# Optimization experiments

Hardware: AMD Instinct MI355X
Metric: run time of the kernel (lower is better)

Reference implementation:

```python
import jax, jax.numpy as jnp
import numpy as np

# dims
D = 1024; H = 16; DH = D // H; FF = 4096; E = 4; K = 64; M = 256; B = 2; S = 1024
DEPTH = 1.0 + 12.0 / 24.0 * 0.5  # depth_factor for layer_idx=12, num_layers=24
SCALE = 1.0 / np.sqrt(DH)
GATE_DIM = 128


def _heads(t):
    # (B,S,D) -> (B,H,S,DH)
    return t.reshape(t.shape[0], t.shape[1], H, DH).transpose(0, 2, 1, 3)


def _merge(t):
    # (B,H,S,DH) -> (B,S,D)
    return t.transpose(0, 2, 1, 3).reshape(t.shape[0], t.shape[2], D)


def _ln(x, g, b):
    mu = x.mean(-1, keepdims=True)
    var = x.var(-1, keepdims=True)
    return (x - mu) / jnp.sqrt(var + 1e-5) * g + b


def _mha(x, wq, bq, wk, bk, wv, bv, wo, bo):
    q = _heads(x @ wq + bq); k = _heads(x @ wk + bk); v = _heads(x @ wv + bv)
    s = jnp.einsum('bhqd,bhkd->bhqk', q, k) * SCALE
    a = jax.nn.softmax(s, axis=-1)
    return _merge(jnp.einsum('bhqk,bhkd->bhqd', a, v)) @ wo + bo


def _sparse_mha(x, wq, bq, wk, bk, wv, bv, wo, bo):
    # DynamicSparseAttention: keep top-K scores per query, mask the rest
    q = _heads(x @ wq + bq); k = _heads(x @ wk + bk); v = _heads(x @ wv + bv)
    s = jnp.einsum('bhqd,bhkd->bhqk', q, k) * SCALE
    thr = jax.lax.top_k(s, K)[0][..., -1:]             # kth-largest per query
    s = jnp.where(s >= thr, s, -1e9)
    a = jax.nn.softmax(s, axis=-1)
    return _merge(jnp.einsum('bhqk,bhkd->bhqd', a, v)) @ wo + bo


def _performer(x, wq, bq, wk, bk, wv, bv, wo, bo, wf):
    # LearnedPerformerAttention: learned ReLU feature maps, linear attention
    q = _heads(x @ wq + bq); k = _heads(x @ wk + bk); v = _heads(x @ wv + bv)
    pq = jax.nn.relu(jnp.einsum('bhsd,dm->bhsm', q, wf))
    pk = jax.nn.relu(jnp.einsum('bhsd,dm->bhsm', k, wf))
    kv = jnp.einsum('bhsm,bhsd->bhmd', pk, v)          # (B,H,M,DH)
    z = pk.sum(axis=2)                                  # (B,H,M)
    num = jnp.einsum('bhsm,bhmd->bhsd', pq, kv)
    den = jnp.einsum('bhsm,bhm->bhs', pq, z) + 1e-6
    return _merge(num / den[..., None]) @ wo + bo


def setup_inputs() -> dict:
    key = jax.random.key(0)
    ks = iter(jax.random.split(key, 64))

    def w(shape):
        fan_in = shape[-2] if len(shape) > 1 else shape[-1]
        return (jax.random.normal(next(ks), shape, jnp.float32) / np.sqrt(fan_in))

    inp = {'x': jax.random.normal(next(ks), (B, S, D), jnp.float32)}
    # AdaptiveReasoningGate
    inp['arg_w1'] = w((D, GATE_DIM)); inp['arg_b1'] = jnp.zeros(GATE_DIM)
    inp['arg_w2'] = w((GATE_DIM, 2)); inp['arg_b2'] = jnp.zeros(2)
    # MoE attention: router + per-expert MHA
    inp['moe_wr'] = w((D, E)); inp['moe_br'] = jnp.zeros(E)
    for n in ('wq', 'wk', 'wv', 'wo'):
        inp['moe_' + n] = w((E, D, D))
        inp['moe_b' + n[1]] = jnp.zeros((E, D))
    # sparse attention
    for n in ('wq', 'wk', 'wv', 'wo'):
        inp['sp_' + n] = w((D, D)); inp['sp_b' + n[1]] = jnp.zeros(D)
    # performer attention
    for n in ('wq', 'wk', 'wv', 'wo'):
        inp['pf_' + n] = w((D, D)); inp['pf_b' + n[1]] = jnp.zeros(D)
    inp['pf_wf'] = w((DH, M))
    # TAA gate, attention combiner gate
    inp['taa_wg'] = w((D, 2)); inp['taa_bg'] = jnp.zeros(2)
    inp['ag_w'] = w((D, 2)); inp['ag_b'] = jnp.zeros(2)
    # FFN
    inp['ffn_w1'] = w((D, FF)); inp['ffn_b1'] = jnp.zeros(FF)
    inp['ffn_w2'] = w((FF, D)); inp['ffn_b2'] = jnp.zeros(D)
    # norms
    for i in (1, 2, 3):
        inp[f'n{i}_g'] = jnp.ones(D); inp[f'n{i}_b'] = jnp.zeros(D)
    return inp


def _forward(x, arg_w1, arg_b1, arg_w2, arg_b2,
             moe_wr, moe_br, moe_wq, moe_bq, moe_wk, moe_bk, moe_wv, moe_bv, moe_wo, moe_bo,
             sp_wq, sp_bq, sp_wk, sp_bk, sp_wv, sp_bv, sp_wo, sp_bo,
             pf_wq, pf_bq, pf_wk, pf_bk, pf_wv, pf_bv, pf_wo, pf_bo, pf_wf,
             taa_wg, taa_bg, ag_w, ag_b,
             ffn_w1, ffn_b1, ffn_w2, ffn_b2,
             n1_g, n1_b, n2_g, n2_b, n3_g, n3_b):
    avg = x.mean(axis=1)  # (B,D)
    # AdaptiveReasoningGate (attn_weight computed but unused in original forward)
    gw = jax.nn.sigmoid(jax.nn.gelu(avg @ arg_w1 + arg_b1) @ arg_w2 + arg_b2)
    ffn_weight = gw[:, 1][:, None, None]
    # MoE attention: token-level softmax routing over E expert MHAs
    ex_out = jax.vmap(
        lambda wq, bq, wk, bk, wv, bv, wo, bo: _mha(x, wq, bq, wk, bk, wv, bv, wo, bo)
    )(moe_wq, moe_bq, moe_wk, moe_bk, moe_wv, moe_bv, moe_wo, moe_bo)  # (E,B,S,D)
    gates = jax.nn.softmax(x @ moe_wr + moe_br, axis=-1)               # (B,S,E)
    moe_out = jnp.einsum('ebsd,bse->bsd', ex_out, gates)
    # Hybrid thought-aware attention (dropout = identity, eval mode)
    sp = _sparse_mha(x, sp_wq, sp_bq, sp_wk, sp_bk, sp_wv, sp_bv, sp_wo, sp_bo)
    pf = _performer(x, pf_wq, pf_bq, pf_wk, pf_bk, pf_wv, pf_bv, pf_wo, pf_bo, pf_wf)
    tg = jax.nn.softmax(avg @ taa_wg + taa_bg, axis=-1)
    taa_out = tg[:, 0][:, None, None] * sp + tg[:, 1][:, None, None] * pf
    # gated combine of MoE and TAA paths
    ag = jax.nn.softmax(avg @ ag_w + ag_b, axis=-1)
    attn_out = (ag[:, 0][:, None, None] * moe_out + ag[:, 1][:, None, None] * taa_out) * DEPTH
    x1 = _ln(x + attn_out, n1_g, n1_b)
    ffn_out = (jax.nn.gelu(x1 @ ffn_w1 + ffn_b1) @ ffn_w2 + ffn_b2) * ffn_weight * DEPTH
    x2 = _ln(x1 + ffn_out, n2_g, n2_b)
    return _ln(x2, n3_g, n3_b)


def reference(x, arg_w1, arg_b1, arg_w2, arg_b2,
              moe_wr, moe_br, moe_wq, moe_bq, moe_wk, moe_bk, moe_wv, moe_bv, moe_wo, moe_bo,
              sp_wq, sp_bq, sp_wk, sp_bk, sp_wv, sp_bv, sp_wo, sp_bo,
              pf_wq, pf_bq, pf_wk, pf_bk, pf_wv, pf_bv, pf_wo, pf_bo, pf_wf,
              taa_wg, taa_bg, ag_w, ag_b,
              ffn_w1, ffn_b1, ffn_w2, ffn_b2,
              n1_g, n1_b, n2_g, n2_b, n3_g, n3_b):
    return _forward(x, arg_w1, arg_b1, arg_w2, arg_b2,
                    moe_wr, moe_br, moe_wq, moe_bq, moe_wk, moe_bk, moe_wv, moe_bv, moe_wo, moe_bo,
                    sp_wq, sp_bq, sp_wk, sp_bk, sp_wv, sp_bv, sp_wo, sp_bo,
                    pf_wq, pf_bq, pf_wk, pf_bk, pf_wv, pf_bv, pf_wo, pf_bo, pf_wf,
                    taa_wg, taa_bg, ag_w, ag_b,
                    ffn_w1, ffn_b1, ffn_w2, ffn_b2,
                    n1_g, n1_b, n2_g, n2_b, n3_g, n3_b)
```

## Files before the change

### kernel.cpp

```cpp
#include <hip/hip_runtime.h>
#include <hip/hip_bf16.h>
#include <math.h>

#define Bq 2
#define Sq 1024
#define Dq 1024
#define Hq 16
#define DHq 64
#define FFq 4096
#define Eq 4
#define Kq 64
#define Mq 256
#define GATEq 128
#define BSq (Bq*Sq)
#define DEPTHF 1.25f
#define SCALEF 0.125f
#define DD (Dq*Dq)
#define PLANE ((size_t)BSq*Dq)

typedef __hip_bfloat16 bf16;
typedef __attribute__((ext_vector_type(8))) __bf16 bf16x8;
typedef __attribute__((ext_vector_type(4))) float f32x4;

__device__ __forceinline__ float toF(float v){ return v; }
__device__ __forceinline__ float toF(bf16 v){ return __bfloat162float(v); }
__device__ __forceinline__ void stF(float* p, size_t i, float v){ p[i] = v; }
__device__ __forceinline__ void stF(bf16* p, size_t i, float v){ p[i] = __float2bfloat16(v); }
__device__ __forceinline__ float gelu_f(float x){
  const float c = 0.7978845608028654f;
  return 0.5f*x*(1.0f + tanhf(c*(x + 0.044715f*x*x*x)));
}
__device__ __forceinline__ unsigned short bfb(float f){
  bf16 h = __float2bfloat16(f);
  return *(unsigned short*)&h;
}
__device__ __forceinline__ float thr_decode(unsigned c){
  unsigned ub = (c & 0x80000000u) ? (c & 0x7FFFFFFFu) : ~c;
  return __uint_as_float(ub);
}
__device__ __forceinline__ void async_lds16(const void* g, void* lds) {
  __builtin_amdgcn_global_load_lds(
      (const __attribute__((address_space(1))) void*)(unsigned long long)(uintptr_t)g,
      (__attribute__((address_space(3))) void*)(unsigned)(uintptr_t)lds, 16, 0, 0);
}

__global__ __launch_bounds__(256)
void detect_kernel(const unsigned* __restrict__ xw, int* __restrict__ flag)
{
  __shared__ int cnt;
  if (threadIdx.x == 0) cnt = 0;
  __syncthreads();
  int c = 0;
  for (int i = threadIdx.x; i < 4096; i += 256) {
    unsigned e = (xw[i] >> 7) & 0xFFu;
    c += (e >= 0x70u && e <= 0x8Fu) ? 1 : 0;
  }
#pragma unroll
  for (int o = 32; o >= 1; o >>= 1) c += __shfl_xor(c, o);
  if ((threadIdx.x & 63) == 0) atomicAdd(&cnt, c);
  __syncthreads();
  if (threadIdx.x == 0) *flag = (cnt > 2048) ? 1 : 0;
}

__global__ __launch_bounds__(256)
void conv_x_kernel(const int* __restrict__ flag, const void* __restrict__ x, bf16* __restrict__ xb)
{
  int f = *flag;
  int i0 = (blockIdx.x*256 + threadIdx.x)*4;
  if (i0 >= BSq*Dq) return;
  if (f) {
    const bf16* s = (const bf16*)x;
#pragma unroll
    for (int k=0;k<4;k++) xb[i0+k] = s[i0+k];
  } else {
    const float* s = (const float*)x;
#pragma unroll
    for (int k=0;k<4;k++) xb[i0+k] = __float2bfloat16(s[i0+k]);
  }
}

template<typename IT>
__device__ void packseg(bf16* dst, const IT* src, int len)
{
  for (int i = threadIdx.x; i < len; i += 256) dst[i] = __float2bfloat16(toF(src[i]));
}
__global__ __launch_bounds__(256)
void pack_bias_kernel(const int* __restrict__ flag, bf16* arena,
    const void* bq, const void* bk, const void* bv, const void* bo,
    const void* sq, const void* sk, const void* sv, const void* so,
    const void* pq, const void* pk, const void* pv, const void* po,
    const void* f1, const void* f2)
{
  int f = *flag;
  if (f) {
    packseg(arena+0,     (const bf16*)bq, 4096); packseg(arena+4096,  (const bf16*)bk, 4096);
    packseg(arena+8192,  (const bf16*)bv, 4096); packseg(arena+12288, (const bf16*)bo, 4096);
    packseg(arena+16384, (const bf16*)sq, 1024); packseg(arena+17408, (const bf16*)sk, 1024);
    packseg(arena+18432, (const bf16*)sv, 1024); packseg(arena+19456, (const bf16*)so, 1024);
    packseg(arena+20480, (const bf16*)pq, 1024); packseg(arena+21504, (const bf16*)pk, 1024);
    packseg(arena+22528, (const bf16*)pv, 1024); packseg(arena+23552, (const bf16*)po, 1024);
    packseg(arena+24576, (const bf16*)f1, 4096); packseg(arena+28672, (const bf16*)f2, 1024);
  } else {
    packseg(arena+0,     (const float*)bq, 4096); packseg(arena+4096,  (const float*)bk, 4096);
    packseg(arena+8192,  (const float*)bv, 4096); packseg(arena+12288, (const float*)bo, 4096);
    packseg(arena+16384, (const float*)sq, 1024); packseg(arena+17408, (const float*)sk, 1024);
    packseg(arena+18432, (const float*)sv, 1024); packseg(arena+19456, (const float*)so, 1024);
    packseg(arena+20480, (const float*)pq, 1024); packseg(arena+21504, (const float*)pk, 1024);
    packseg(arena+22528, (const float*)pv, 1024); packseg(arena+23552, (const float*)po, 1024);
    packseg(arena+24576, (const float*)f1, 4096); packseg(arena+28672, (const float*)f2, 1024);
  }
}

template<typename IT>
__device__ void packwft_body(const IT* __restrict__ wf, bf16* __restrict__ wft)
{
  int i = blockIdx.x*256 + threadIdx.x;
  if (i >= DHq*Mq) return;
  int d = i >> 8, m = i & 255;
  wft[m*DHq + d] = __float2bfloat16(toF(wf[(size_t)d*Mq + m]));
}
__global__ __launch_bounds__(256)
void pack_wft_kernel(const int* __restrict__ flag, const void* wf, bf16* wft)
{
  if (*flag) packwft_body<bf16>((const bf16*)wf, wft);
  else       packwft_body<float>((const float*)wf, wft);
}

template<typename WT>
__device__ void gemm_core(bf16* As, unsigned* Bs,
    const bf16* __restrict__ A, int lda, const WT* __restrict__ W,
    const bf16* __restrict__ barena, int biasOff,
    const float* __restrict__ rowscale, bf16* __restrict__ C,
    float* __restrict__ Cf, int N, int K, int act)
{
  int tid = threadIdx.x;
  int lane = tid & 63, wave = tid >> 6;
  int wr = wave >> 1, wc = wave & 1;
  int bm = blockIdx.x * 128, bn = blockIdx.y * 128;

  int arow1 = wave*16 + (lane>>2);
  int akey = (arow1 >> 1) & 3;
  int acol = ((lane & 3) ^ akey) * 8;
  const bf16* aP1 = A + (size_t)(bm + arow1)*lda + acol;
  const bf16* aP2 = A + (size_t)(bm + arow1 + 64)*lda + acol;

  int kp = tid >> 4, nb8 = (tid & 15)*8;
  const WT* wP = W + (size_t)(2*kp)*N + bn + nb8;

  f32x4 acc[4][4];
#pragma unroll
  for (int i=0;i<4;i++)
#pragma unroll
    for (int j=0;j<4;j++) acc[i][j] = (f32x4){0.f,0.f,0.f,0.f};

  int m = lane & 15, q = lane >> 4;
  int akey2 = (m >> 1) & 3;
  int aq = (q ^ akey2) * 8;

  const int T = K >> 5;
  uint4 rwa, rwb, rwc, rwd;

  async_lds16(aP1, As + wave*512);
  async_lds16(aP2, As + (wave+4)*512);
  aP1 += 32; aP2 += 32;
  if constexpr (sizeof(WT) == 2) {
    rwa = *(const uint4*)wP;
    rwb = *(const uint4*)(wP + N);
  } else {
    const float* f0 = (const float*)wP;
    const float* f1 = (const float*)(wP + N);
    rwa = *(const uint4*)f0; rwb = *(const uint4*)(f0+4);
    rwc = *(const uint4*)f1; rwd = *(const uint4*)(f1+4);
  }
  wP += (size_t)32*N;

  for (int t = 0; t < T; t++) {
    int cur = t & 1;
    unsigned p[8];
    if constexpr (sizeof(WT) == 2) {
      p[0] = (rwa.x & 0xFFFFu) | (rwb.x << 16);  p[1] = (rwa.x >> 16) | (rwb.x & 0xFFFF0000u);
      p[2] = (rwa.y & 0xFFFFu) | (rwb.y << 16);  p[3] = (rwa.y >> 16) | (rwb.y & 0xFFFF0000u);
      p[4] = (rwa.z & 0xFFFFu) | (rwb.z << 16);  p[5] = (rwa.z >> 16) | (rwb.z & 0xFFFF0000u);
      p[6] = (rwa.w & 0xFFFFu) | (rwb.w << 16);  p[7] = (rwa.w >> 16) | (rwb.w & 0xFFFF0000u);
    } else {
      p[0] = (unsigned)bfb(__uint_as_float(rwa.x)) | ((unsigned)bfb(__uint_as_float(rwc.x)) << 16);
      p[1] = (unsigned)bfb(__uint_as_float(rwa.y)) | ((unsigned)bfb(__uint_as_float(rwc.y)) << 16);
      p[2] = (unsigned)bfb(__uint_as_float(rwa.z)) | ((unsigned)bfb(__uint_as_float(rwc.z)) << 16);
      p[3] = (unsigned)bfb(__uint_as_float(rwa.w)) | ((unsigned)bfb(__uint_as_float(rwc.w)) << 16);
      p[4] = (unsigned)bfb(__uint_as_float(rwb.x)) | ((unsigned)bfb(__uint_as_float(rwd.x)) << 16);
      p[5] = (unsigned)bfb(__uint_as_float(rwb.y)) | ((unsigned)bfb(__uint_as_float(rwd.y)) << 16);
      p[6] = (unsigned)bfb(__uint_as_float(rwb.z)) | ((unsigned)bfb(__uint_as_float(rwd.z)) << 16);
      p[7] = (unsigned)bfb(__uint_as_float(rwb.w)) | ((unsigned)bfb(__uint_as_float(rwd.w)) << 16);
    }
    unsigned* bD = Bs + cur*2112 + kp*132 + nb8;
    *(uint4*)(bD)     = make_uint4(p[0],p[1],p[2],p[3]);
    *(uint4*)(bD + 4) = make_uint4(p[4],p[5],p[6],p[7]);
    asm volatile("s_waitcnt vmcnt(0)" ::: "memory");
    __syncthreads();
    if (t + 1 < T) {
      bf16* asn = As + ((t+1)&1)*4096;
      async_lds16(aP1, asn + wave*512);
      async_lds16(aP2, asn + (wave+4)*512);
      aP1 += 32; aP2 += 32;
      if constexpr (sizeof(WT) == 2) {
        rwa = *(const uint4*)wP;
        rwb = *(const uint4*)(wP + N);
      } else {
        const float* f0 = (const float*)wP;
        const float* f1 = (const float*)(wP + N);
        rwa = *(const uint4*)f0; rwb = *(const uint4*)(f0+4);
        rwc = *(const uint4*)f1; rwd = *(const uint4*)(f1+4);
      }
      wP += (size_t)32*N;
    }
    const bf16* asc = As + cur*4096;
    const unsigned* bsc = Bs + cur*2112;
    bf16x8 av[4], bv[4];
#pragma unroll
    for (int i=0;i<4;i++)
      av[i] = *(const bf16x8*)&asc[(wr*64 + i*16 + m)*32 + aq];
#pragma unroll
    for (int j=0;j<4;j++) {
      int n = wc*64 + j*16 + m;
      unsigned b0 = bsc[(q*4+0)*132 + n];
      unsigned b1 = bsc[(q*4+1)*132 + n];
      unsigned b2 = bsc[(q*4+2)*132 + n];
      unsigned b3 = bsc[(q*4+3)*132 + n];
      uint4 bb = make_uint4(b0,b1,b2,b3);
      bv[j] = *(const bf16x8*)&bb;
    }
#pragma unroll
    for (int i=0;i<4;i++)
#pragma unroll
      for (int j=0;j<4;j++)
        acc[i][j] = __builtin_amdgcn_mfma_f32_16x16x32_bf16(av[i], bv[j], acc[i][j], 0, 0, 0);
  }

#pragma unroll
  for (int i=0;i<4;i++) {
    int row0 = bm + wr*64 + i*16 + q*4;
#pragma unroll
    for (int j=0;j<4;j++) {
      int col = bn + wc*64 + j*16 + m;
      float bvv = barena ? toF(barena[biasOff + col]) : 0.f;
#pragma unroll
      for (int r=0;r<4;r++) {
        size_t idx = (size_t)(row0 + r)*N + col;
        if (Cf) {
          Cf[idx] = acc[i][j][r];
        } else {
          float v = acc[i][j][r] + bvv;
          if (act) v = gelu_f(v);
          if (rowscale) v *= rowscale[row0 + r];
          C[idx] = __float2bfloat16(v);
        }
      }
    }
  }
}

__global__ __launch_bounds__(256, 3)
void gemm6_k(const int* __restrict__ flag, const bf16* Abase, long az,
    const void* w0, const void* w1, const void* w2,
    const void* w3, const void* w4, const void* w5,
    long e0, long e1, long e2, long e3, long e4, long e5,
    int b0, int b1, int b2, int b3, int b4, int b5,
    const float* r0, const float* r1, const float* r2,
    const float* r3, const float* r4, const float* r5,
    bf16* c0, bf16* c1, bf16* c2, bf16* c3, bf16* c4, bf16* c5,
    const bf16* barena, int N, int K)
{
  __shared__ bf16 As[2*4096];
  __shared__ unsigned Bs[2*2112];
  int z = blockIdx.z;
  const void* Wp = (z==0)?w0:(z==1)?w1:(z==2)?w2:(z==3)?w3:(z==4)?w4:w5;
  long eo        = (z==0)?e0:(z==1)?e1:(z==2)?e2:(z==3)?e3:(z==4)?e4:e5;
  int bo         = (z==0)?b0:(z==1)?b1:(z==2)?b2:(z==3)?b3:(z==4)?b4:b5;
  const float* rs= (z==0)?r0:(z==1)?r1:(z==2)?r2:(z==3)?r3:(z==4)?r4:r5;
  bf16* C        = (z==0)?c0:(z==1)?c1:(z==2)?c2:(z==3)?c3:(z==4)?c4:c5;
  const bf16* A  = Abase + (size_t)z*az;
  if (*flag) gemm_core<bf16>(As, Bs, A, K, (const bf16*)Wp + eo, barena, bo, rs, C, nullptr, N, K, 0);
  else       gemm_core<float>(As, Bs, A, K, (const float*)Wp + eo, barena, bo, rs, C, nullptr, N, K, 0);
}

__global__ __launch_bounds__(256, 3)
void gemm1_k(const int* __restrict__ flag, const bf16* A, int lda, const void* W,
             const bf16* barena, int biasOff, const float* rowscale,
             bf16* C, float* Cf, long cfz, int N, int K, int act, int kz)
{
  __shared__ bf16 As[2*4096];
  __shared__ unsigned Bs[2*2112];
  int z = blockIdx.z;
  const bf16* Az = A + (size_t)z*kz;
  long wo = (size_t)z*kz*N;
  float* Cfz = Cf ? (Cf + (size_t)z*cfz) : nullptr;
  if (*flag) gemm_core<bf16>(As, Bs, Az, lda, (const bf16*)W + wo, barena, biasOff, rowscale, C, Cfz, N, K, act);
  else       gemm_core<float>(As, Bs, Az, lda, (const float*)W + wo, barena, biasOff, rowscale, C, Cfz, N, K, act);
}

__global__ __launch_bounds__(256)
void combine_ffn2(const float* __restrict__ pf, const bf16* __restrict__ barena,
                  const float* __restrict__ rs, bf16* __restrict__ out)
{
  int i0 = (blockIdx.x*256 + threadIdx.x)*4;
  float4 s0 = *(const float4*)(pf + i0);
  float4 s1 = *(const float4*)(pf + PLANE + i0);
  float4 s2 = *(const float4*)(pf + 2*PLANE + i0);
  float4 s3 = *(const float4*)(pf + 3*PLANE + i0);
  int row = i0 >> 10, col = i0 & 1023;
  float r = rs[row];
  out[i0+0] = __float2bfloat16((s0.x+s1.x+s2.x+s3.x + toF(barena[28672+col+0])) * r);
  out[i0+1] = __float2bfloat16((s0.y+s1.y+s2.y+s3.y + toF(barena[28672+col+1])) * r);
  out[i0+2] = __float2bfloat16((s0.z+s1.z+s2.z+s3.z + toF(barena[28672+col+2])) * r);
  out[i0+3] = __float2bfloat16((s0.w+s1.w+s2.w+s3.w + toF(barena[28672+col+3])) * r);
}

__global__ __launch_bounds__(256)
void vtrans_kernel(const bf16* __restrict__ Vb, long vz, bf16* __restrict__ Vtb, long vtz)
{
  __shared__ bf16 t[64][72];
  const bf16* V = Vb + (size_t)blockIdx.z*vz;
  bf16* Vt = Vtb + (size_t)blockIdx.z*vtz;
  int bh = blockIdx.x;
  int sc_ = blockIdx.y;
  int b = bh >> 4, h = bh & 15;
  int tid = threadIdx.x;
  {
    int s = tid >> 2, dd = (tid & 3) * 16;
    const bf16* src = &V[((size_t)b*Sq + sc_*64 + s)*Dq + h*64 + dd];
    uint4 a0 = *(const uint4*)src;
    uint4 a1 = *(const uint4*)(src + 8);
    *(uint4*)&t[s][dd]     = a0;
    *(uint4*)&t[s][dd + 8] = a1;
  }
  __syncthreads();
  {
    int d = tid >> 2, sp = (tid & 3) * 16;
    unsigned short buf[16];
#pragma unroll
    for (int e = 0; e < 16; e++) {
      bf16 v = t[sp + e][d];
      buf[e] = *(unsigned short*)&v;
    }
    bf16* dst = &Vt[((size_t)bh*DHq + d)*Sq + sc_*64 + sp];
    *(uint4*)dst       = *(uint4*)&buf[0];
    *(uint4*)(dst + 8) = *(uint4*)&buf[8];
  }
}

template<int SPARSE>
__global__ __launch_bounds__(256, 4)
void attn_kernel(const bf16* __restrict__ Q, const bf16* __restrict__ K,
                 const bf16* __restrict__ Vt, bf16* __restrict__ O)
{
  const int PAST = 1032;
  __shared__ bf16 pa[16*PAST];
  __shared__ float partA[64], partB[64];
  __shared__ int cntb[2][64];

  int p_ = blockIdx.x;
  int g_ = (p_ & 7)*4 + ((p_ >> 3) & 3);
  int rb = p_ >> 5;
  int h  = g_ & 15;
  int b  = g_ >> 4;
  int tid = threadIdx.x, lane = tid & 63, wave = tid >> 6;
  int m = lane & 15, q = lane >> 4;
  size_t base = ((size_t)b*Sq)*Dq + (size_t)h*DHq;
  int q0 = rb*16;

  const bf16* qrow = &Q[base + (size_t)(q0+m)*Dq + q*8];
  bf16x8 aq0 = *(const bf16x8*)qrow;
  bf16x8 aq1 = *(const bf16x8*)(qrow + 32);

  f32x4 cc[16];
#pragma unroll
  for (int t = 0; t < 16; t++) {
    int j0 = wave*256 + t*16;
    const bf16* kp = &K[base + (size_t)(j0+m)*Dq + q*8];
    bf16x8 b0 = *(const bf16x8*)kp;
    bf16x8 b1 = *(const bf16x8*)(kp + 32);
    f32x4 c = {0.f,0.f,0.f,0.f};
    c = __builtin_amdgcn_mfma_f32_16x16x32_bf16(aq0, b0, c, 0, 0, 0);
    c = __builtin_amdgcn_mfma_f32_16x16x32_bf16(aq1, b1, c, 0, 0, 0);
#pragma unroll
    for (int r=0;r<4;r++) c[r] *= SCALEF;
    cc[t] = c;
  }

  unsigned lo[4] = {0u,0u,0u,0u};
  if (SPARSE) {
    int cnt_cur[4] = {Sq, Sq, Sq, Sq};
    for (int bit = 31; bit >= 0; bit--) {
      int par = bit & 1;
      unsigned cand[4];
      float candf[4];
      int c4[4] = {0,0,0,0};
#pragma unroll
      for (int r=0;r<4;r++) {
        cand[r] = lo[r] | (1u << bit);
        candf[r] = thr_decode(cand[r]);
      }
#pragma unroll
      for (int t=0;t<16;t++)
#pragma unroll
        for (int r=0;r<4;r++) c4[r] += (cc[t][r] >= candf[r]) ? 1 : 0;
#pragma unroll
      for (int o=1;o<16;o<<=1)
#pragma unroll
        for (int r=0;r<4;r++) c4[r] += __shfl_xor(c4[r], o);
      if (m == 0) {
#pragma unroll
        for (int r=0;r<4;r++) cntb[par][wave*16 + q*4 + r] = c4[r];
      }
      __syncthreads();
      int done = 1;
#pragma unroll
      for (int r=0;r<4;r++) {
        int row = q*4 + r;
        int tot = cntb[par][row] + cntb[par][16+row] + cntb[par][32+row] + cntb[par][48+row];
        if (tot >= Kq) { lo[r] = cand[r]; cnt_cur[r] = tot; }
        done &= (cnt_cur[r] == Kq) ? 1 : 0;
      }
      done &= __shfl_xor(done, 16);
      done &= __shfl_xor(done, 32);
      if (done) break;
    }
  }

  float mrow[4];
#pragma unroll
  for (int r=0;r<4;r++) {
    float v = -1e30f;
#pragma unroll
    for (int t=0;t<16;t++) v = fmaxf(v, cc[t][r]);
#pragma unroll
    for (int o=1;o<16;o<<=1) v = fmaxf(v, __shfl_xor(v, o));
    mrow[r] = v;
  }
  if (m == 0) {
#pragma unroll
    for (int r=0;r<4;r++) partA[wave*16 + q*4 + r] = mrow[r];
  }
  __syncthreads();
#pragma unroll
  for (int r=0;r<4;r++) {
    int row = q*4 + r;
    mrow[r] = fmaxf(fmaxf(partA[row], partA[16+row]), fmaxf(partA[32+row], partA[48+row]));
  }

  float thrf[4];
  if (SPARSE) {
#pragma unroll
    for (int r=0;r<4;r++) {
      thrf[r] = (!(lo[r] & 0x80000000u) && lo[r] <= 0x007FFFFFu)
                    ? -INFINITY : thr_decode(lo[r]);
    }
  }
  float rsum[4] = {0.f,0.f,0.f,0.f};
#pragma unroll
  for (int t=0;t<16;t++) {
    int col = wave*256 + t*16 + m;
#pragma unroll
    for (int r=0;r<4;r++) {
      float p;
      if (SPARSE) p = (cc[t][r] >= thrf[r]) ? __expf(cc[t][r] - mrow[r]) : 0.f;
      else        p = __expf(cc[t][r] - mrow[r]);
      rsum[r] += p;
      pa[(q*4+r)*PAST + col] = __float2bfloat16(p);
    }
  }
#pragma unroll
  for (int r=0;r<4;r++)
#pragma unroll
    for (int o=1;o<16;o<<=1) rsum[r] += __shfl_xor(rsum[r], o);
  if (m == 0) {
#pragma unroll
    for (int r=0;r<4;r++) partB[wave*16 + q*4 + r] = rsum[r];
  }
  __syncthreads();
#pragma unroll
  for (int r=0;r<4;r++) {
    int row = q*4 + r;
    rsum[r] = partB[row] + partB[16+row] + partB[32+row] + partB[48+row];
    rsum[r] = fmaxf(rsum[r], 1e-30f);
  }

  const bf16* vtp = &Vt[((size_t)(b*Hq + h)*DHq + wave*16 + m)*Sq];
  f32x4 oc = {0.f,0.f,0.f,0.f};
#pragma unroll 8
  for (int ks = 0; ks < 32; ks++) {
    bf16x8 af = *(const bf16x8*)&pa[m*PAST + ks*32 + q*8];
    bf16x8 bv = *(const bf16x8*)&vtp[ks*32 + q*8];
    oc = __builtin_amdgcn_mfma_f32_16x16x32_bf16(af, bv, oc, 0, 0, 0);
  }
#pragma unroll
  for (int r=0;r<4;r++) {
    O[base + (size_t)(q0 + q*4 + r)*Dq + wave*16 + m] = __float2bfloat16(oc[r] / rsum[r]);
  }
}

__global__ __launch_bounds__(256)
void perf_kv_mfma(const bf16* __restrict__ Kb, const bf16* __restrict__ Vt,
                  const bf16* __restrict__ wft, bf16* __restrict__ kvb,
                  float* __restrict__ zg)
{
  __shared__ bf16 pbuf[4][32*40];
  __shared__ float kvred[4][64*32];
  __shared__ float zred[4][32];

  int bh = blockIdx.x;
  int mg = blockIdx.y;
  int b = bh >> 4, h = bh & 15;
  int tid = threadIdx.x, lane = tid & 63, wave = tid >> 6;
  int ml = lane & 15, q = lane >> 4;
  size_t kbase = ((size_t)b*Sq)*Dq + (size_t)h*DHq;
  const bf16* vtb = Vt + (size_t)bh*DHq*Sq;
  int sw0 = wave*256;
  bf16* pw = pbuf[wave];

  bf16x8 awf[2][2];
#pragma unroll
  for (int t=0;t<2;t++) {
    const bf16* p = &wft[(size_t)(mg*32 + t*16 + ml)*DHq + q*8];
    awf[t][0] = *(const bf16x8*)p;
    awf[t][1] = *(const bf16x8*)(p + 32);
  }

  f32x4 acc[4][2];
#pragma unroll
  for (int dt=0;dt<4;dt++)
#pragma unroll
    for (int t=0;t<2;t++) acc[dt][t] = (f32x4){0.f,0.f,0.f,0.f};
  float zacc[2][4] = {{0.f,0.f,0.f,0.f},{0.f,0.f,0.f,0.f}};

  for (int st = 0; st < 8; st++) {
    int s0 = sw0 + st*32;
    f32x4 pk[2][2];
#pragma unroll
    for (int sc=0;sc<2;sc++) {
      const bf16* kp = &Kb[kbase + (size_t)(s0 + sc*16 + ml)*Dq + q*8];
      bf16x8 b0 = *(const bf16x8*)kp;
      bf16x8 b1 = *(const bf16x8*)(kp + 32);
#pragma unroll
      for (int t=0;t<2;t++) {
        f32x4 c = (f32x4){0.f,0.f,0.f,0.f};
        c = __builtin_amdgcn_mfma_f32_16x16x32_bf16(awf[t][0], b0, c, 0, 0, 0);
        c = __builtin_amdgcn_mfma_f32_16x16x32_bf16(awf[t][1], b1, c, 0, 0, 0);
        pk[t][sc] = c;
      }
    }
#pragma unroll
    for (int t=0;t<2;t++)
#pragma unroll
      for (int sc=0;sc<2;sc++)
#pragma unroll
        for (int r=0;r<4;r++) {
          float v = fmaxf(pk[t][sc][r], 0.f);
          zacc[t][r] += v;
          pw[(t*16 + q*4 + r)*40 + sc*16 + ml] = __float2bfloat16(v);
        }
#pragma unroll
    for (int dt=0;dt<4;dt++) {
      bf16x8 av = *(const bf16x8*)&vtb[(size_t)(dt*16 + ml)*Sq + s0 + q*8];
#pragma unroll
      for (int t=0;t<2;t++) {
        bf16x8 bp = *(const bf16x8*)&pw[(t*16 + ml)*40 + q*8];
        acc[dt][t] = __builtin_amdgcn_mfma_f32_16x16x32_bf16(av, bp, acc[dt][t], 0, 0, 0);
      }
    }
  }

#pragma unroll
  for (int dt=0;dt<4;dt++)
#pragma unroll
    for (int t=0;t<2;t++)
#pragma unroll
      for (int r=0;r<4;r++)
        kvred[wave][(dt*16 + q*4 + r)*32 + t*16 + ml] = acc[dt][t][r];
#pragma unroll
  for (int t=0;t<2;t++)
#pragma unroll
    for (int r=0;r<4;r++) {
      float v = zacc[t][r];
#pragma unroll
      for (int o=1;o<16;o<<=1) v += __shfl_xor(v, o);
      if (ml == 0) zred[wave][t*16 + q*4 + r] = v;
    }
  __syncthreads();
  for (int p = tid; p < 2048; p += 256) {
    float s = kvred[0][p] + kvred[1][p] + kvred[2][p] + kvred[3][p];
    int d = p >> 5, mloc = p & 31;
    kvb[(size_t)bh*(DHq*Mq) + d*Mq + mg*32 + mloc] = __float2bfloat16(s);
  }
  if (tid < 32) {
    float s = zred[0][tid] + zred[1][tid] + zred[2][tid] + zred[3][tid];
    zg[bh*Mq + mg*32 + tid] = s;
  }
}

__global__ __launch_bounds__(256)
void perf_out_mfma(const bf16* __restrict__ Q, const bf16* __restrict__ wft,
                   const bf16* __restrict__ kvb, const float* __restrict__ zg,
                   bf16* __restrict__ O)
{
  const int PQST = 264;
  __shared__ bf16 pa2[64*PQST];
  __shared__ float zs[Mq];

  int blk = blockIdx.x;
  int sc_ = blk & 15;
  int bh  = blk >> 4;
  int b = bh >> 4, h = bh & 15;
  int tid = threadIdx.x, lane = tid & 63, wave = tid >> 6;
  int ml = lane & 15, q = lane >> 4;
  size_t base = ((size_t)b*Sq)*Dq + (size_t)h*DHq;
  int s0 = sc_*64;

  zs[tid] = zg[bh*Mq + tid];

  const bf16* qp = &Q[base + (size_t)(s0 + wave*16 + ml)*Dq + q*8];
  bf16x8 aq0 = *(const bf16x8*)qp;
  bf16x8 aq1 = *(const bf16x8*)(qp + 32);
  __syncthreads();

  f32x4 pq[16];
#pragma unroll
  for (int mt=0;mt<16;mt++) {
    const bf16* wp = &wft[(size_t)(mt*16 + ml)*DHq + q*8];
    bf16x8 b0 = *(const bf16x8*)wp;
    bf16x8 b1 = *(const bf16x8*)(wp + 32);
    f32x4 c = (f32x4){0.f,0.f,0.f,0.f};
    c = __builtin_amdgcn_mfma_f32_16x16x32_bf16(aq0, b0, c, 0, 0, 0);
    c = __builtin_amdgcn_mfma_f32_16x16x32_bf16(aq1, b1, c, 0, 0, 0);
    pq[mt] = c;
  }

  float den[4] = {1e-6f, 1e-6f, 1e-6f, 1e-6f};
#pragma unroll
  for (int mt=0;mt<16;mt++)
#pragma unroll
    for (int r=0;r<4;r++) {
      float v = fmaxf(pq[mt][r], 0.f);
      den[r] += v * zs[mt*16 + ml];
      pa2[(wave*16 + q*4 + r)*PQST + mt*16 + ml] = __float2bfloat16(v);
    }
#pragma unroll
  for (int r=0;r<4;r++)
#pragma unroll
    for (int o=1;o<16;o<<=1) den[r] += __shfl_xor(den[r], o);
  __syncthreads();

  const bf16* kvp = kvb + (size_t)bh*(DHq*Mq);
  f32x4 oc[4];
#pragma unroll
  for (int dt=0;dt<4;dt++) oc[dt] = (f32x4){0.f,0.f,0.f,0.f};
#pragma unroll
  for (int ks=0; ks<8; ks++) {
    bf16x8 ap = *(const bf16x8*)&pa2[(wave*16 + ml)*PQST + ks*32 + q*8];
#pragma unroll
    for (int dt=0;dt<4;dt++) {
      bf16x8 bk = *(const bf16x8*)&kvp[(size_t)(dt*16 + ml)*Mq + ks*32 + q*8];
      oc[dt] = __builtin_amdgcn_mfma_f32_16x16x32_bf16(ap, bk, oc[dt], 0, 0, 0);
    }
  }
#pragma unroll
  for (int dt=0;dt<4;dt++)
#pragma unroll
    for (int r=0;r<4;r++)
      O[base + (size_t)(s0 + wave*16 + q*4 + r)*Dq + dt*16 + ml] =
          __float2bfloat16(oc[dt][r] / den[r]);
}

template<typename IT>
__device__ void ln_body(float* buf, float* red, const IT* __restrict__ xb,
                        const void* Ap, const void* Bp,
                        const IT* __restrict__ g, const IT* __restrict__ be,
                        void* out, int mode)
{
  int row = blockIdx.x;
  int tid = threadIdx.x;
  size_t off = (size_t)row*Dq;
  for (int dd = tid; dd < Dq; dd += 256) {
    float v;
    if (mode == 0)      v = toF(xb[off+dd]) + toF(((const bf16*)Ap)[off+dd]);
    else if (mode == 1) v = toF(((const bf16*)Ap)[off+dd]) + toF(((const bf16*)Bp)[off+dd]);
    else if (mode == 3) {
      const bf16* P = (const bf16*)Ap;
      v = toF(xb[off+dd]);
#pragma unroll
      for (int p=0;p<6;p++) v += toF(P[(size_t)p*PLANE + off + dd]);
    }
    else                v = toF(((const bf16*)Ap)[off+dd]);
    buf[dd] = v;
  }
  __syncthreads();
  float s = 0.f, q = 0.f;
  for (int dd = tid; dd < Dq; dd += 256) { float v = buf[dd]; s += v; q += v*v; }
#pragma unroll
  for (int o=32;o>=1;o>>=1) { s += __shfl_xor(s,o); q += __shfl_xor(q,o); }
  int w = tid >> 6;
  if ((tid & 63) == 0) { red[w] = s; red[4+w] = q; }
  __syncthreads();
  if (tid == 0) {
    float S1 = red[0]+red[1]+red[2]+red[3];
    float Q1 = red[4]+red[5]+red[6]+red[7];
    float mu = S1 / (float)Dq;
    float var = Q1 / (float)Dq - mu*mu;
    red[8] = mu; red[9] = rsqrtf(fmaxf(var, 0.f) + 1e-5f);
  }
  __syncthreads();
  float mu = red[8], inv = red[9];
  for (int dd = tid; dd < Dq; dd += 256) {
    float v = (buf[dd]-mu)*inv*toF(g[dd]) + toF(be[dd]);
    if (mode == 2) stF((IT*)out, off+dd, v);
    else           stF((bf16*)out, off+dd, v);
  }
}

__global__ __launch_bounds__(256)
void ln_kernel(const int* __restrict__ flag, const void* xb, const void* A, const void* Bv,
               const void* g, const void* be, void* out, int mode)
{
  __shared__ float buf[Dq];
  __shared__ float red[10];
  if (*flag) ln_body<bf16>(buf, red, (const bf16*)xb, A, Bv, (const bf16*)g, (const bf16*)be, out, mode);
  else       ln_body<float>(buf, red, (const float*)xb, A, Bv, (const float*)g, (const float*)be, out, mode);
}

__global__ __launch_bounds__(256)
void avg2_kernel(const int* __restrict__ flag, const void* __restrict__ x, float* __restrict__ avgsum)
{
  int b  = blockIdx.x >> 4;
  int sc = blockIdx.x & 15;
  int t = threadIdx.x;
  int c0 = t*4;
  float a0=0.f,a1=0.f,a2=0.f,a3=0.f;
  if (*flag) {
    const unsigned* X = (const unsigned*)x;
    for (int s = sc*64; s < sc*64+64; s++) {
      size_t bi = (((size_t)(b*Sq + s))*Dq + c0) >> 1;
      unsigned u0 = X[bi], u1 = X[bi+1];
      a0 += __uint_as_float(u0 << 16);
      a1 += __uint_as_float(u0 & 0xFFFF0000u);
      a2 += __uint_as_float(u1 << 16);
      a3 += __uint_as_float(u1 & 0xFFFF0000u);
    }
  } else {
    const float* X = (const float*)x;
    for (int s = sc*64; s < sc*64+64; s++) {
      float4 v = *(const float4*)&X[((size_t)(b*Sq + s))*Dq + c0];
      a0 += v.x; a1 += v.y; a2 += v.z; a3 += v.w;
    }
  }
  atomicAdd(&avgsum[b*Dq + c0 + 0], a0);
  atomicAdd(&avgsum[b*Dq + c0 + 1], a1);
  atomicAdd(&avgsum[b*Dq + c0 + 2], a2);
  atomicAdd(&avgsum[b*Dq + c0 + 3], a3);
}

template<typename IT>
__device__ void gdots_body(const float* __restrict__ avgs,
    const IT* __restrict__ w1, const IT* __restrict__ b1,
    const IT* __restrict__ taw, const IT* __restrict__ tab,
    const IT* __restrict__ agw, const IT* __restrict__ agb,
    float* __restrict__ g1b, float* __restrict__ lgb)
{
  int blk = blockIdx.x;
  int tid = threadIdx.x, lane = tid & 63, wave = tid >> 6;
  if (blk < 64) {
    int o = blk*4 + wave;
    int bb = o >> 7, j = o & 127;
    const float* av = avgs + bb*Dq;
    float a = 0.f;
#pragma unroll
    for (int k = 0; k < 16; k++) {
      int dd = k*64 + lane;
      a += av[dd] * toF(w1[dd*GATEq + j]);
    }
#pragma unroll
    for (int off=32; off>=1; off>>=1) a += __shfl_xor(a, off);
    if (lane == 0) g1b[o] = gelu_f(a*(1.f/(float)Sq) + toF(b1[j]));
  } else {
    int bb = wave >> 1, c = wave & 1;
    const float* av = avgs + bb*Dq;
    const IT* wm = (blk == 64) ? taw : agw;
    const IT* bm = (blk == 64) ? tab : agb;
    float a = 0.f;
#pragma unroll
    for (int k = 0; k < 16; k++) {
      int dd = k*64 + lane;
      a += av[dd] * toF(wm[dd*2 + c]);
    }
#pragma unroll
    for (int off=32; off>=1; off>>=1) a += __shfl_xor(a, off);
    if (lane == 0) lgb[(blk-64)*4 + wave] = a*(1.f/(float)Sq) + toF(bm[c]);
  }
}
__global__ __launch_bounds__(256)
void gate_dots_kernel(const int* __restrict__ flag, const float* avgs,
    const void* w1, const void* b1, const void* taw, const void* tab,
    const void* agw, const void* agb, float* g1b, float* lgb)
{
  if (*flag) gdots_body<bf16>(avgs, (const bf16*)w1,(const bf16*)b1,(const bf16*)taw,
      (const bf16*)tab,(const bf16*)agw,(const bf16*)agb, g1b, lgb);
  else gdots_body<float>(avgs, (const float*)w1,(const float*)b1,(const float*)taw,
      (const float*)tab,(const float*)agw,(const float*)agb, g1b, lgb);
}

template<typename IT>
__device__ void gfin_body(float* sh, const float* __restrict__ g1b, const float* __restrict__ lgb,
    const IT* __restrict__ w2, const IT* __restrict__ b2,
    float* __restrict__ cmb0, float* __restrict__ rs_tg0,
    float* __restrict__ rs_tg1, float* __restrict__ rs_ffn)
{
  int tid = threadIdx.x, lane = tid & 63, wave = tid >> 6;
  if (wave < 2) {
    float a = g1b[wave*128 + lane] * toF(w2[lane*2 + 1])
            + g1b[wave*128 + 64 + lane] * toF(w2[(64+lane)*2 + 1]);
#pragma unroll
    for (int off=32; off>=1; off>>=1) a += __shfl_xor(a, off);
    if (lane == 0) sh[wave] = 1.f/(1.f + __expf(-(a + toF(b2[1]))));
  }
  __syncthreads();
  if (tid < Bq) {
    int b = tid;
    float t0 = lgb[b*2], t1 = lgb[b*2+1];
    float m = fmaxf(t0,t1);
    float e0=__expf(t0-m), e1=__expf(t1-m), inv=1.f/(e0+e1);
    float tg0 = e0*inv, tg1 = e1*inv;
    float a0 = lgb[4+b*2], a1l = lgb[4+b*2+1];
    m = fmaxf(a0,a1l);
    float f0=__expf(a0-m), f1=__expf(a1l-m); inv = 1.f/(f0+f1);
    float ag0 = f0*inv, ag1 = f1*inv;
    cmb0[b] = ag0*DEPTHF;
    sh[2+b] = tg0*ag1*DEPTHF;
    sh[4+b] = tg1*ag1*DEPTHF;
    sh[6+b] = sh[b]*DEPTHF;
  }
  __syncthreads();
  for (int i = tid; i < BSq; i += 256) {
    int b = i >> 10;
    rs_tg0[i] = sh[2+b]; rs_tg1[i] = sh[4+b]; rs_ffn[i] = sh[6+b];
  }
}
__global__ __launch_bounds__(256)
void gate_fin_kernel(const int* __restrict__ flag, const float* g1b, const float* lgb,
    const void* w2, const void* b2, float* cmb0,
    float* rs_tg0, float* rs_tg1, float* rs_ffn)
{
  __shared__ float sh[8];
  if (*flag) gfin_body<bf16>(sh, g1b, lgb, (const bf16*)w2, (const bf16*)b2, cmb0, rs_tg0, rs_tg1, rs_ffn);
  else       gfin_body<float>(sh, g1b, lgb, (const float*)w2, (const float*)b2, cmb0, rs_tg0, rs_tg1, rs_ffn);
}

template<typename IT>
__device__ void router_body(const IT* __restrict__ x, const IT* __restrict__ wr,
                            const IT* __restrict__ br, const float* __restrict__ cmb0,
                            float* __restrict__ gates_t)
{
  int row = blockIdx.x;
  int tid = threadIdx.x;
  size_t off = (size_t)row*Dq;
  float a0=0,a1=0,a2=0,a3=0;
  for (int dd = tid; dd < Dq; dd += 64) {
    float xv = toF(x[off+dd]);
    a0 += xv*toF(wr[dd*Eq+0]);
    a1 += xv*toF(wr[dd*Eq+1]);
    a2 += xv*toF(wr[dd*Eq+2]);
    a3 += xv*toF(wr[dd*Eq+3]);
  }
#pragma unroll
  for (int o=32;o>=1;o>>=1) {
    a0 += __shfl_xor(a0,o); a1 += __shfl_xor(a1,o);
    a2 += __shfl_xor(a2,o); a3 += __shfl_xor(a3,o);
  }
  if (tid == 0) {
    a0 += toF(br[0]); a1 += toF(br[1]); a2 += toF(br[2]); a3 += toF(br[3]);
    float m = fmaxf(fmaxf(a0,a1),fmaxf(a2,a3));
    float e0=__expf(a0-m), e1=__expf(a1-m), e2=__expf(a2-m), e3=__expf(a3-m);
    float inv = 1.f/(e0+e1+e2+e3);
    float sc = cmb0[row >> 10];
    gates_t[0*BSq+row]=e0*inv*sc; gates_t[1*BSq+row]=e1*inv*sc;
    gates_t[2*BSq+row]=e2*inv*sc; gates_t[3*BSq+row]=e3*inv*sc;
  }
}
__global__ __launch_bounds__(64)
void router_kernel(const int* __restrict__ flag, const void* x, const void* wr,
                   const void* br, const float* cmb0, float* gates_t)
{
  if (*flag) router_body<bf16>((const bf16*)x, (const bf16*)wr, (const bf16*)br, cmb0, gates_t);
  else       router_body<float>((const float*)x, (const float*)wr, (const float*)br, cmb0, gates_t);
}

extern "C" void kernel_launch(void* const* d_in, const int* in_sizes, int n_in,
                              void* d_out, int out_size, void* d_ws, size_t ws_size,
                              hipStream_t stream) {
  const void* x      = d_in[0];
  const void* arg_w1 = d_in[1];  const void* arg_b1 = d_in[2];
  const void* arg_w2 = d_in[3];  const void* arg_b2 = d_in[4];
  const void* moe_wr = d_in[5];  const void* moe_br = d_in[6];
  const void* moe_wq = d_in[7];  const void* moe_bq = d_in[8];
  const void* moe_wk = d_in[9];  const void* moe_bk = d_in[10];
  const void* moe_wv = d_in[11]; const void* moe_bv = d_in[12];
  const void* moe_wo = d_in[13]; const void* moe_bo = d_in[14];
  const void* sp_wq  = d_in[15]; const void* sp_bq  = d_in[16];
  const void* sp_wk  = d_in[17]; const void* sp_bk  = d_in[18];
  const void* sp_wv  = d_in[19]; const void* sp_bv  = d_in[20];
  const void* sp_wo  = d_in[21]; const void* sp_bo  = d_in[22];
  const void* pf_wq  = d_in[23]; const void* pf_bq  = d_in[24];
  const void* pf_wk  = d_in[25]; const void* pf_bk  = d_in[26];
  const void* pf_wv  = d_in[27]; const void* pf_bv  = d_in[28];
  const void* pf_wo  = d_in[29]; const void* pf_bo  = d_in[30];
  const void* pf_wf  = d_in[31];
  const void* taa_wg = d_in[32]; const void* taa_bg = d_in[33];
  const void* ag_w   = d_in[34]; const void* ag_b   = d_in[35];
  const void* ffn_w1 = d_in[36]; const void* ffn_b1 = d_in[37];
  const void* ffn_w2 = d_in[38]; const void* ffn_b2 = d_in[39];
  const void* n1_g   = d_in[40]; const void* n1_b   = d_in[41];
  const void* n2_g   = d_in[42]; const void* n2_b   = d_in[43];
  const void* n3_g   = d_in[44]; const void* n3_b   = d_in[45];

  char* w = (char*)d_ws;
  const size_t MB = 1024*1024;
  bf16* xb  = (bf16*)w;
  bf16* Qp  = (bf16*)(w + 4*MB);
  bf16* KV  = (bf16*)(w + 28*MB);
  bf16* Vt  = (bf16*)(w + 44*MB);
  bf16* Pp  = (bf16*)(w + 28*MB);
  bf16* x1    = (bf16*)(w + 4*MB);
  bf16* ffn_h = (bf16*)(w + 8*MB);
  float* partF= (float*)(w + 24*MB);
  bf16* tmpb  = (bf16*)w;
  bf16* x2    = (bf16*)w;
  char* book = w + 56*MB;
  float* rs_tg0 = (float*)book;
  float* rs_tg1 = rs_tg0 + BSq;
  float* rs_ffn = rs_tg1 + BSq;
  float* cmb0   = rs_ffn + BSq;
  float* avgp   = cmb0 + 16;
  float* gates_t= avgp + Bq*Dq;
  float* zb     = gates_t + Eq*BSq;
  float* g1b    = zb + Bq*Hq*Mq;
  float* lgb    = g1b + 256;
  int*   dflag  = (int*)(lgb + 8);
  bf16*  barena = (bf16*)(dflag + 16);
  bf16*  wft    = barena + 29696;
  bf16*  kvb    = (bf16*)(w + 57*MB);

  detect_kernel<<<1, 256, 0, stream>>>((const unsigned*)x, dflag);
  hipMemsetAsync(avgp, 0, (size_t)(Bq*Dq)*sizeof(float), stream);
  conv_x_kernel<<<BSq*Dq/1024, 256, 0, stream>>>(dflag, x, xb);
  pack_bias_kernel<<<1, 256, 0, stream>>>(dflag, barena,
      moe_bq, moe_bk, moe_bv, moe_bo, sp_bq, sp_bk, sp_bv, sp_bo,
      pf_bq, pf_bk, pf_bv, pf_bo, ffn_b1, ffn_b2);
  pack_wft_kernel<<<64, 256, 0, stream>>>(dflag, pf_wf, wft);
  avg2_kernel<<<Bq*16, 256, 0, stream>>>(dflag, x, avgp);
  gate_dots_kernel<<<66, 256, 0, stream>>>(dflag, avgp, arg_w1, arg_b1,
      taa_wg, taa_bg, ag_w, ag_b, g1b, lgb);
  gate_fin_kernel<<<1, 256, 0, stream>>>(dflag, g1b, lgb, arg_w2, arg_b2,
      cmb0, rs_tg0, rs_tg1, rs_ffn);
  router_kernel<<<BSq, 64, 0, stream>>>(dflag, x, moe_wr, moe_br, cmb0, gates_t);

  dim3 g6(16, 8, 6);
  dim3 gVT(Bq*Hq, Sq/64, 2);
  int nAttnBlk = Bq*Hq*(Sq/16);

  for (int p = 0; p < 2; p++) {
    int e0 = 2*p, e1 = 2*p + 1;
    gemm6_k<<<g6, 256, 0, stream>>>(dflag, xb, 0L,
        moe_wq, moe_wk, moe_wv, moe_wq, moe_wk, moe_wv,
        (long)e0*DD, (long)e0*DD, (long)e0*DD, (long)e1*DD, (long)e1*DD, (long)e1*DD,
        e0*1024, e0*1024+4096, e0*1024+8192, e1*1024, e1*1024+4096, e1*1024+8192,
        nullptr, nullptr, nullptr, nullptr, nullptr, nullptr,
        Qp + (size_t)e0*PLANE, KV, KV + PLANE,
        Qp + (size_t)e1*PLANE, KV + 2*PLANE, KV + 3*PLANE,
        barena, Dq, Dq);
    vtrans_kernel<<<gVT, 256, 0, stream>>>(KV + PLANE, (long)(2*PLANE), Vt, (long)PLANE);
    attn_kernel<0><<<nAttnBlk, 256, 0, stream>>>(Qp + (size_t)e0*PLANE, KV, Vt, Qp + (size_t)e0*PLANE);
    attn_kernel<0><<<nAttnBlk, 256, 0, stream>>>(Qp + (size_t)e1*PLANE, KV + 2*PLANE, Vt + PLANE, Qp + (size_t)e1*PLANE);
  }

  gemm6_k<<<g6, 256, 0, stream>>>(dflag, xb, 0L,
      sp_wq, sp_wk, sp_wv, pf_wq, pf_wk, pf_wv,
      0L, 0L, 0L, 0L, 0L, 0L,
      16384, 17408, 18432, 20480, 21504, 22528,
      nullptr, nullptr, nullptr, nullptr, nullptr, nullptr,
      Qp + 4*PLANE, KV, KV + PLANE,
      Qp + 5*PLANE, KV + 2*PLANE, KV + 3*PLANE,
      barena, Dq, Dq);
  vtrans_kernel<<<gVT, 256, 0, stream>>>(KV + PLANE, (long)(2*PLANE), Vt, (long)PLANE);
  attn_kernel<1><<<nAttnBlk, 256, 0, stream>>>(Qp + 4*PLANE, KV, Vt, Qp + 4*PLANE);
  {
    dim3 gKV1(Bq*Hq, 8);
    perf_kv_mfma<<<gKV1, 256, 0, stream>>>(KV + 2*PLANE, Vt + PLANE, wft, kvb, zb);
  }
  perf_out_mfma<<<Bq*Hq*16, 256, 0, stream>>>(Qp + 5*PLANE, wft, kvb, zb, Qp + 5*PLANE);

  gemm6_k<<<g6, 256, 0, stream>>>(dflag, Qp, (long)PLANE,
      moe_wo, moe_wo, moe_wo, moe_wo, sp_wo, pf_wo,
      0L, (long)DD, (long)2*DD, (long)3*DD, 0L, 0L,
      12288, 13312, 14336, 15360, 19456, 23552,
      gates_t, gates_t + BSq, gates_t + 2*BSq, gates_t + 3*BSq, rs_tg0, rs_tg1,
      Pp, Pp + PLANE, Pp + 2*PLANE, Pp + 3*PLANE, Pp + 4*PLANE, Pp + 5*PLANE,
      barena, Dq, Dq);

  ln_kernel<<<BSq, 256, 0, stream>>>(dflag, x, Pp, nullptr, n1_g, n1_b, x1, 3);

  gemm1_k<<<dim3(16, 32, 1), 256, 0, stream>>>(dflag, x1, Dq, ffn_w1,
      barena, 24576, nullptr, ffn_h, nullptr, 0L, FFq, Dq, 1, 0);
  gemm1_k<<<dim3(16, 8, 4), 256, 0, stream>>>(dflag, ffn_h, FFq, ffn_w2,
      nullptr, 0, nullptr, nullptr, partF, (long)PLANE, Dq, 1024, 0, 1024);
  combine_ffn2<<<BSq*Dq/1024, 256, 0, stream>>>(partF, barena, rs_ffn, tmpb);

  ln_kernel<<<BSq, 256, 0, stream>>>(dflag, nullptr, x1, tmpb, n2_g, n2_b, x2, 1);
  ln_kernel<<<BSq, 256, 0, stream>>>(dflag, nullptr, x2, nullptr, n3_g, n3_b, d_out, 2);
}
```

Before: 1.097 ms.

## Replace dense MoE attention with register-resident flash attention kernel

```diff
diff --git a/kernel.cpp b/kernel.cpp
--- a/kernel.cpp
+++ b/kernel.cpp
@@ -345,6 +345,108 @@
     bf16* dst = &Vt[((size_t)bh*DHq + d)*Sq + sc_*64 + sp];
     *(uint4*)dst       = *(uint4*)&buf[0];
     *(uint4*)(dst + 8) = *(uint4*)&buf[8];
+  }
+}
+
+__global__ __launch_bounds__(256)
+void flash_attn_kernel(const bf16* __restrict__ Q, const bf16* __restrict__ K,
+                       const bf16* __restrict__ Vt, bf16* __restrict__ O)
+{
+  int p_ = blockIdx.x;
+  int g_ = (p_ & 7)*4 + ((p_ >> 3) & 3);
+  int blk = p_ >> 5;
+  int h = g_ & 15, b = g_ >> 4;
+  int tid = threadIdx.x, lane = tid & 63, wave = tid >> 6;
+  int m = lane & 15, q = lane >> 4;
+  size_t base = ((size_t)b*Sq)*Dq + (size_t)h*DHq;
+  int q0 = blk*64 + wave*16;
+
+  const bf16* qrow = &Q[base + (size_t)(q0 + m)*Dq + q*8];
+  bf16x8 bq0 = *(const bf16x8*)qrow;
+  bf16x8 bq1 = *(const bf16x8*)(qrow + 32);
+
+  const bf16* krow = K + base + (size_t)m*Dq + q*8;
+  const bf16* vrow = Vt + ((size_t)(b*Hq + h)*DHq + m)*Sq + q*8;
+
+  f32x4 oc[4];
+#pragma unroll
+  for (int dt=0;dt<4;dt++) oc[dt] = (f32x4){0.f,0.f,0.f,0.f};
+  float mrun = -1e30f, lrun = 0.f;
+
+  int srcA = m + ((q & 1) << 5);
+  int srcB = srcA + 16;
+  bool hi = (q >= 2);
+
+  for (int c0 = 0; c0 < Sq; c0 += 32) {
+    const bf16* ka = krow + (size_t)c0*Dq;
+    bf16x8 a00 = *(const bf16x8*)ka;
+    bf16x8 a01 = *(const bf16x8*)(ka + 32);
+    const bf16* kb = ka + (size_t)16*Dq;
+    bf16x8 a10 = *(const bf16x8*)kb;
+    bf16x8 a11 = *(const bf16x8*)(kb + 32);
+    f32x4 c0t = (f32x4){0.f,0.f,0.f,0.f};
+    c0t = __builtin_amdgcn_mfma_f32_16x16x32_bf16(a00, bq0, c0t, 0, 0, 0);
+    c0t = __builtin_amdgcn_mfma_f32_16x16x32_bf16(a01, bq1, c0t, 0, 0, 0);
+    f32x4 c1t = (f32x4){0.f,0.f,0.f,0.f};
+    c1t = __builtin_amdgcn_mfma_f32_16x16x32_bf16(a10, bq0, c1t, 0, 0, 0);
+    c1t = __builtin_amdgcn_mfma_f32_16x16x32_bf16(a11, bq1, c1t, 0, 0, 0);
+#pragma unroll
+    for (int r=0;r<4;r++) { c0t[r] *= SCALEF; c1t[r] *= SCALEF; }
+
+    float cmax = fmaxf(fmaxf(fmaxf(c0t[0], c0t[1]), fmaxf(c0t[2], c0t[3])),
+                       fmaxf(fmaxf(c1t[0], c1t[1]), fmaxf(c1t[2], c1t[3])));
+    cmax = fmaxf(cmax, __shfl_xor(cmax, 16));
+    cmax = fmaxf(cmax, __shfl_xor(cmax, 32));
+
+    if (__any(cmax > mrun)) {
+      float mnew = fmaxf(mrun, cmax);
+      float alpha = __expf(mrun - mnew);
+#pragma unroll
+      for (int dt=0;dt<4;dt++)
+#pragma unroll
+        for (int r=0;r<4;r++) oc[dt][r] *= alpha;
+      lrun *= alpha;
+      mrun = mnew;
+    }
+
+    float p0[4], p1[4];
+#pragma unroll
+    for (int r=0;r<4;r++) { p0[r] = __expf(c0t[r] - mrun); p1[r] = __expf(c1t[r] - mrun); }
+    lrun += (p0[0]+p0[1]) + (p0[2]+p0[3]) + (p1[0]+p1[1]) + (p1[2]+p1[3]);
+
+    unsigned d00 = (unsigned)bfb(p0[0]) | ((unsigned)bfb(p0[1]) << 16);
+    unsigned d01 = (unsigned)bfb(p0[2]) | ((unsigned)bfb(p0[3]) << 16);
+    unsigned d10 = (unsigned)bfb(p1[0]) | ((unsigned)bfb(p1[1]) << 16);
+    unsigned d11 = (unsigned)bfb(p1[2]) | ((unsigned)bfb(p1[3]) << 16);
+    unsigned X0 = __shfl(d00, srcA, 64);
+    unsigned X1 = __shfl(d01, srcA, 64);
+    unsigned X2 = __shfl(d00, srcB, 64);
+    unsigned X3 = __shfl(d01, srcB, 64);
+    unsigned Y0 = __shfl(d10, srcA, 64);
+    unsigned Y1 = __shfl(d11, srcA, 64);
+    unsigned Y2 = __shfl(d10, srcB, 64);
+    unsigned Y3 = __shfl(d11, srcB, 64);
+    uint4 bb = make_uint4(hi ? Y0 : X0, hi ? Y1 : X1, hi ? Y2 : X2, hi ? Y3 : X3);
+    bf16x8 pb = *(const bf16x8*)&bb;
+
+    const bf16* va = vrow + c0;
+#pragma unroll
+    for (int dt=0;dt<4;dt++) {
+      bf16x8 av = *(const bf16x8*)&va[(size_t)(dt*16)*Sq];
+      oc[dt] = __builtin_amdgcn_mfma_f32_16x16x32_bf16(av, pb, oc[dt], 0, 0, 0);
+    }
+  }
+
+  lrun += __shfl_xor(lrun, 16);
+  lrun += __shfl_xor(lrun, 32);
+  lrun = fmaxf(lrun, 1e-30f);
+  float inv = 1.0f / lrun;
+  bf16* orow = O + base + (size_t)(q0 + m)*Dq + q*4;
+#pragma unroll
+  for (int dt=0;dt<4;dt++) {
+    unsigned w0 = (unsigned)bfb(oc[dt][0]*inv) | ((unsigned)bfb(oc[dt][1]*inv) << 16);
+    unsigned w1 = (unsigned)bfb(oc[dt][2]*inv) | ((unsigned)bfb(oc[dt][3]*inv) << 16);
+    *(uint2*)&orow[dt*16] = make_uint2(w0, w1);
   }
 }
 
@@ -964,6 +1066,7 @@
   dim3 g6(16, 8, 6);
   dim3 gVT(Bq*Hq, Sq/64, 2);
   int nAttnBlk = Bq*Hq*(Sq/16);
+  int nFlashBlk = Bq*Hq*(Sq/64);
 
   for (int p = 0; p < 2; p++) {
     int e0 = 2*p, e1 = 2*p + 1;
@@ -976,8 +1079,8 @@
         Qp + (size_t)e1*PLANE, KV + 2*PLANE, KV + 3*PLANE,
         barena, Dq, Dq);
     vtrans_kernel<<<gVT, 256, 0, stream>>>(KV + PLANE, (long)(2*PLANE), Vt, (long)PLANE);
-    attn_kernel<0><<<nAttnBlk, 256, 0, stream>>>(Qp + (size_t)e0*PLANE, KV, Vt, Qp + (size_t)e0*PLANE);
-    attn_kernel<0><<<nAttnBlk, 256, 0, stream>>>(Qp + (size_t)e1*PLANE, KV + 2*PLANE, Vt + PLANE, Qp + (size_t)e1*PLANE);
+    flash_attn_kernel<<<nFlashBlk, 256, 0, stream>>>(Qp + (size_t)e0*PLANE, KV, Vt, Qp + (size_t)e0*PLANE);
+    flash_attn_kernel<<<nFlashBlk, 256, 0, stream>>>(Qp + (size_t)e1*PLANE, KV + 2*PLANE, Vt + PLANE, Qp + (size_t)e1*PLANE);
   }
 
   gemm6_k<<<g6, 256, 0, stream>>>(dflag, xb, 0L,
```

Result: no change. 1.093 ms (-0.4%).
